# Kernel tuning notes

Measured on AMD Instinct MI355X. Metric: run time of the kernel, lower is better.

## Reference

```python
import jax, jax.numpy as jnp
import numpy as np
import math

B, L = 4, 4096
D_MODEL = 1024
D_INNER = 1024          # expand=1
D_STATE = 1             # required by rearrange 'b d 1 l' in ssm()
D_CONV = 2
DT_RANK = 64            # ceil(1024/16)
EPS = 1e-5


def setup_inputs() -> dict:
    key = jax.random.key(0)
    ks = jax.random.split(key, 8)
    dt_min, dt_max, dt_floor = 1e-3, 1e-1, 1e-4
    # dt_proj bias init: inverse-softplus of log-uniform dt (faithful to dt_init)
    dt = jnp.exp(jax.random.uniform(ks[5], (D_INNER,)) * (math.log(dt_max) - math.log(dt_min)) + math.log(dt_min))
    dt = jnp.clip(dt, dt_floor, None)
    inv_dt = dt + jnp.log(-jnp.expm1(-dt))
    std = DT_RANK ** -0.5
    return {
        "x": jax.random.normal(ks[0], (B, L, D_MODEL), dtype=jnp.float32),
        "w_in": jax.random.normal(ks[1], (2 * D_INNER, D_MODEL), dtype=jnp.float32) * 0.02,
        "conv_w": jax.random.normal(ks[2], (D_INNER, 1, D_CONV), dtype=jnp.float32) * 0.5,
        "conv_b": jnp.zeros((D_INNER,), dtype=jnp.float32),
        "x_proj_weight": jax.random.normal(ks[3], (DT_RANK + 2 * D_STATE, D_INNER), dtype=jnp.float32) * 0.02,
        "dt_projs_weight": jax.random.uniform(ks[4], (D_INNER, DT_RANK), minval=-std, maxval=std, dtype=jnp.float32),
        "dt_projs_bias": inv_dt,
        "A_logs": jnp.tile(jnp.log(jnp.arange(1, D_STATE + 1, dtype=jnp.float32))[None, :], (D_INNER, 1)),
        "Ds": jnp.ones((D_INNER,), dtype=jnp.float32),
        "ln_w": jnp.ones((D_INNER,), dtype=jnp.float32),
        "ln_b": jnp.zeros((D_INNER,), dtype=jnp.float32),
        "w_out": jax.random.normal(ks[6], (D_MODEL, D_INNER), dtype=jnp.float32) * 0.02,
    }


def _selective_scan(u, delta, A, Bs):
    # u, delta: (B, D, L); A: (D, N); Bs: (B, N, L) -> hidden states h: (B, D, N, L)
    dA = jnp.exp(jnp.einsum('bdl,dn->bdnl', delta, A))            # (B,D,N,L)
    dBu = jnp.einsum('bdl,bnl,bdl->bdnl', delta, Bs, u)           # delta * B * u
    dA_t = jnp.moveaxis(dA, -1, 0)                                # (L,B,D,N)
    dBu_t = jnp.moveaxis(dBu, -1, 0)

    def step(h, inp):
        a_t, bu_t = inp
        h = a_t * h + bu_t
        return h, h

    h0 = jnp.zeros(dA.shape[:-1], dtype=u.dtype)
    _, hs = jax.lax.scan(step, h0, (dA_t, dBu_t))                 # (L,B,D,N)
    return jnp.moveaxis(hs, 0, -1)                                # (B,D,N,L)


def reference(x, w_in, conv_w, conv_b, x_proj_weight, dt_projs_weight,
              dt_projs_bias, A_logs, Ds, ln_w, ln_b, w_out):
    Bsz, Lsz, _ = x.shape
    # in_proj (bias=False), chunk into x and gate z
    xz = x @ w_in.T                                               # (B,L,2*D)
    xc, z = xz[..., :D_INNER], xz[..., D_INNER:]
    xc = jnp.transpose(xc, (0, 2, 1))                             # (B,D,L)
    # depthwise causal conv1d, padding=d_conv-1, truncated to L
    xc = jax.lax.conv_general_dilated(
        xc, conv_w, window_strides=(1,), padding=[(D_CONV - 1, D_CONV - 1)],
        feature_group_count=D_INNER,
        dimension_numbers=('NCH', 'OIH', 'NCH'))[..., :Lsz]
    xc = xc + conv_b[None, :, None]
    xc = jax.nn.silu(xc)
    # ssm()
    x_dbl = jnp.einsum('rd,bdl->brl', x_proj_weight, xc)          # (B,R+2N,L)
    dts = x_dbl[:, :DT_RANK]
    Bs = x_dbl[:, DT_RANK:DT_RANK + D_STATE]                      # (B,N,L)
    Cs = x_dbl[:, DT_RANK + D_STATE:]                             # (B,N,L)
    dts = jnp.einsum('dr,brl->bdl', dt_projs_weight, dts)         # (B,D,L)
    A = -jnp.exp(A_logs)                                          # (D,N)
    delta = jax.nn.softplus(dts + dt_projs_bias[None, :, None])   # delta_softplus=True
    h = _selective_scan(xc, delta, A, Bs)                         # (B,D,N,L)
    h = h.reshape(Bsz, D_INNER * D_STATE, Lsz)                    # 'b d 1 l -> b (d 1) l' (N==1)
    y = h * Cs + xc * Ds[:, None]                                 # (B,D,L)
    # out_norm (LayerNorm over d_inner), gate, out_proj
    y = jnp.transpose(y, (0, 2, 1))                               # (B,L,D)
    mu = jnp.mean(y, axis=-1, keepdims=True)
    var = jnp.mean(jnp.square(y - mu), axis=-1, keepdims=True)
    y = (y - mu) * jax.lax.rsqrt(var + EPS) * ln_w + ln_b
    y = y * jax.nn.silu(z)
    return y @ w_out.T                                            # (B,L,d_model)
```

## Files before the change

kernel.cpp:

```cpp
#include <hip/hip_runtime.h>
#include <hip/hip_bf16.h>
#include <cstdint>
#include <cstddef>

typedef short short8 __attribute__((ext_vector_type(8)));
typedef short short4v __attribute__((ext_vector_type(4)));
typedef float floatx4 __attribute__((ext_vector_type(4)));

constexpr int Bz = 4;
constexpr int Lz = 4096;
constexpr int Dm = 1024;
constexpr int Di = 1024;
constexpr int Mrows = Bz * Lz;
constexpr int CH  = 32;
constexpr int NCH = Lz / CH;
constexpr int XPJ_KS = 4;

__device__ __forceinline__ void load16(const void* g, void* l) {
  __builtin_amdgcn_global_load_lds((__attribute__((address_space(1))) void*)g,
                                   (__attribute__((address_space(3))) void*)l,
                                   16, 0, 0);
}

__device__ __forceinline__ float bf2f(const __hip_bfloat16 v) { return __bfloat162float(v); }
__device__ __forceinline__ short f2bfs(float v) {
  __hip_bfloat16 h = __float2bfloat16(v);
  return *(short*)&h;
}

__global__ __launch_bounds__(256) void cvt_all(
    const float* __restrict__ x, const float* __restrict__ w_in,
    const float* __restrict__ w_out, const float* __restrict__ xpw,
    const float* __restrict__ dtw,
    __hip_bfloat16* __restrict__ xbf, __hip_bfloat16* __restrict__ w_in_bf,
    __hip_bfloat16* __restrict__ w_out_bf, __hip_bfloat16* __restrict__ xpw_bf,
    __hip_bfloat16* __restrict__ dtw_bf)
{
  const int i = blockIdx.x * 256 + threadIdx.x;
  const float* src; __hip_bfloat16* dst; int j;
  if (i < 4194304)      { src = x;     dst = xbf;      j = i; }
  else if (i < 4718592) { src = w_in;  dst = w_in_bf;  j = i - 4194304; }
  else if (i < 4980736) { src = w_out; dst = w_out_bf; j = i - 4718592; }
  else if (i < 4997632) { src = xpw;   dst = xpw_bf;   j = i - 4980736; }
  else if (i < 5014016) { src = dtw;   dst = dtw_bf;   j = i - 4997632; }
  else return;
  const float4 v = ((const float4*)src)[j];
  short4v s;
  s[0] = f2bfs(v.x); s[1] = f2bfs(v.y); s[2] = f2bfs(v.z); s[3] = f2bfs(v.w);
  ((short4v*)dst)[j] = s;
}

template <int EPI>
__global__ __launch_bounds__(256) void gemm128(
    const __hip_bfloat16* __restrict__ A,
    const __hip_bfloat16* __restrict__ W,
    int K, int N,
    __hip_bfloat16* __restrict__ outb0,
    __hip_bfloat16* __restrict__ outb1,
    float* __restrict__ outf,
    const float* __restrict__ biasf)
{
  constexpr int BK = 32;
  constexpr int GY = 16;
  __shared__ short sA[128 * BK];
  __shared__ short sB[128 * BK];
  const int tid  = threadIdx.x;
  const int wid  = tid >> 6;
  const int lane = tid & 63;

  const int gx  = gridDim.x;
  const int id  = blockIdx.y * gx + blockIdx.x;
  const int seg = gx * GY;
  const int bx  = (id % seg) / GY;
  const int by  = (id / seg) * GY + (id % GY);

  const int m0 = by * 128;
  const int n0 = bx * 128;
  const int wm = (wid & 1) * 64;
  const int wn = (wid >> 1) * 64;

  floatx4 acc[4][4];
#pragma unroll
  for (int i = 0; i < 4; i++)
#pragma unroll
    for (int j = 0; j < 4; j++) acc[i][j] = (floatx4){0.f, 0.f, 0.f, 0.f};

  const short* Ag = (const short*)A + (size_t)(m0 + (tid >> 2)) * K + (tid & 3) * 8;
  const short* Bg = (const short*)W + (size_t)(n0 + (tid >> 2)) * K + (tid & 3) * 8;
  short* sAd = &sA[tid * 8];
  short* sBd = &sB[tid * 8];
  const size_t rstep = (size_t)64 * K;
  const int fr = lane & 15, fq = lane >> 4;

  for (int kb = 0; kb < K; kb += BK) {
    load16(Ag, sAd);
    load16(Ag + rstep, sAd + 2048);
    load16(Bg, sBd);
    load16(Bg + rstep, sBd + 2048);
    Ag += BK; Bg += BK;
    __syncthreads();

    short8 av[4], bv[4];
#pragma unroll
    for (int mt = 0; mt < 4; mt++) av[mt] = *(const short8*)&sA[(wm + mt * 16 + fr) * BK + fq * 8];
#pragma unroll
    for (int nt = 0; nt < 4; nt++) bv[nt] = *(const short8*)&sB[(wn + nt * 16 + fr) * BK + fq * 8];
#pragma unroll
    for (int mt = 0; mt < 4; mt++)
#pragma unroll
      for (int nt = 0; nt < 4; nt++)
        acc[mt][nt] = __builtin_amdgcn_mfma_f32_16x16x32_bf16(av[mt], bv[nt], acc[mt][nt], 0, 0, 0);
    __syncthreads();
  }

#pragma unroll
  for (int mt = 0; mt < 4; mt++) {
#pragma unroll
    for (int nt = 0; nt < 4; nt++) {
#pragma unroll
      for (int r = 0; r < 4; r++) {
        const int gm = m0 + wm + mt * 16 + fq * 4 + r;
        const int gn = n0 + wn + nt * 16 + fr;
        float v = acc[mt][nt][r];
        if constexpr (EPI == 0) {
          if (gn < 1024) outb0[(size_t)gm * 1024 + gn] = __float2bfloat16(v);
          else           outb1[(size_t)gm * 1024 + (gn - 1024)] = __float2bfloat16(v);
        } else if constexpr (EPI == 1) {
          v += biasf[gn];
          v = (v > 15.f) ? v : __logf(1.f + __expf(v));
          outb0[(size_t)gm * N + gn] = __float2bfloat16(v);
        } else {
          outf[(size_t)gm * N + gn] = v;
        }
      }
    }
  }
}

__device__ __forceinline__ void wait_lgkm0() {
  asm volatile("s_waitcnt lgkmcnt(0)");
  __builtin_amdgcn_sched_barrier(0);
}

template <int EPI>
__device__ __forceinline__ void cluster_mfma(int MQ, floatx4 (&acc)[8][4],
                                             const short8 (&av)[8][2],
                                             const short8 (&bv)[4][2])
{
  __builtin_amdgcn_s_setprio(1);
#pragma unroll
  for (int j = 0; j < 2; j++)
#pragma unroll
    for (int nf = 0; nf < 4; nf++)
#pragma unroll
      for (int ks = 0; ks < 2; ks++)
        acc[2 * MQ + j][nf] = __builtin_amdgcn_mfma_f32_16x16x32_bf16(
            av[2 * MQ + j][ks], bv[nf][ks], acc[2 * MQ + j][nf], 0, 0, 0);
  __builtin_amdgcn_s_setprio(0);
}

template <int EPI>
__global__ __launch_bounds__(512, 2) void gemm256(
    const __hip_bfloat16* __restrict__ A,
    const __hip_bfloat16* __restrict__ W,
    int K, int N,
    __hip_bfloat16* __restrict__ outb0,
    __hip_bfloat16* __restrict__ outb1,
    float* __restrict__ outf)
{
  __shared__ alignas(16) char lds[131072];
  const int tid  = threadIdx.x;
  const int wid  = tid >> 6;
  const int lane = tid & 63;
  const int wm = wid >> 2;
  const int wn = wid & 3;
  const int fr = lane & 15, fq = lane >> 4;

  const int gx   = gridDim.x;
  const int nwg  = gx * gridDim.y;
  const int orig = blockIdx.y * gx + blockIdx.x;
  const int swz  = (orig & 7) * (nwg >> 3) + (orig >> 3);
  const int bx   = swz % gx;
  const int by   = swz / gx;
  const int m0 = by * 256;
  const int n0 = bx * 256;
  const size_t K2 = (size_t)K * 2;

  int rowo[2], colo[2];
#pragma unroll
  for (int i = 0; i < 2; i++) {
    const int p = i * 8192 + tid * 16;
    const int s = p >> 10;
    const int r = (p >> 6) & 15;
    rowo[i] = (s >> 1) * 16 + r;
    colo[i] = (s & 1) * 64 + ((p & 63) ^ (((r >> 3) & 1) << 5));
  }
  const char* Ab = (const char*)A + (size_t)m0 * K2;
  const char* Bb = (const char*)W + (size_t)n0 * K2;
  char* lbase = (char*)lds;

#define STAGE_A(c, h, kt) do {                                                          \
    load16(Ab + (size_t)((h) * 128 + rowo[0]) * K2 + (size_t)(kt) * 128 + colo[0],      \
           lbase + (c) * 32768 + (h) * 16384 + tid * 16);                               \
    load16(Ab + (size_t)((h) * 128 + rowo[1]) * K2 + (size_t)(kt) * 128 + colo[1],      \
           lbase + (c) * 32768 + (h) * 16384 + 8192 + tid * 16);                        \
  } while (0)
#define STAGE_B(c, h, kt) do {                                                          \
    load16(Bb + (size_t)((h) * 128 + rowo[0]) * K2 + (size_t)(kt) * 128 + colo[0],      \
           lbase + 65536 + (c) * 32768 + (h) * 16384 + tid * 16);                       \
    load16(Bb + (size_t)((h) * 128 + rowo[1]) * K2 + (size_t)(kt) * 128 + colo[1],      \
           lbase + 65536 + (c) * 32768 + (h) * 16384 + 8192 + tid * 16);                \
  } while (0)

  const int foff = (fr * 64 + fq * 16) ^ (((fr >> 3) & 1) << 5);

  floatx4 acc[8][4];
#pragma unroll
  for (int i = 0; i < 8; i++)
#pragma unroll
    for (int j = 0; j < 4; j++) acc[i][j] = (floatx4){0.f, 0.f, 0.f, 0.f};

  STAGE_A(0, 0, 0); STAGE_A(0, 1, 0); STAGE_B(0, 0, 0); STAGE_B(0, 1, 0);
  STAGE_B(1, 0, 1); STAGE_B(1, 1, 1); STAGE_A(1, 0, 1);
  asm volatile("s_waitcnt vmcnt(6)");
  __builtin_amdgcn_sched_barrier(0);
  __builtin_amdgcn_s_barrier();

  const int NT = K >> 6;
  short8 av[8][2], bv[4][2];
#pragma unroll 2
  for (int t = 0; t < NT; ++t) {
    const int cur = t & 1, nxt = cur ^ 1;
    const char* la = lbase + cur * 32768 + wm * 16384 + foff;
    const char* lb = lbase + 65536 + cur * 32768 + (wn >> 1) * 16384 + (wn & 1) * 8192 + foff;

#pragma unroll
    for (int nf = 0; nf < 4; nf++)
#pragma unroll
      for (int ks = 0; ks < 2; ks++)
        bv[nf][ks] = *(const short8*)(lb + (nf * 2 + ks) * 1024);
#pragma unroll
    for (int mf = 0; mf < 2; mf++)
#pragma unroll
      for (int ks = 0; ks < 2; ks++)
        av[mf][ks] = *(const short8*)(la + (mf * 2 + ks) * 1024);
    if (t + 1 < NT) STAGE_A(nxt, 1, t + 1);
    wait_lgkm0();
    cluster_mfma<EPI>(0, acc, av, bv);
    __builtin_amdgcn_s_barrier();

#pragma unroll
    for (int mf = 2; mf < 4; mf++)
#pragma unroll
      for (int ks = 0; ks < 2; ks++)
        av[mf][ks] = *(const short8*)(la + (mf * 2 + ks) * 1024);
    if (t + 2 < NT) STAGE_B(cur, 0, t + 2);
    wait_lgkm0();
    cluster_mfma<EPI>(1, acc, av, bv);
    __builtin_amdgcn_s_barrier();

#pragma unroll
    for (int mf = 4; mf < 8; mf++)
#pragma unroll
      for (int ks = 0; ks < 2; ks++)
        av[mf][ks] = *(const short8*)(la + (mf * 2 + ks) * 1024);
    if (t + 2 < NT) STAGE_B(cur, 1, t + 2);
    wait_lgkm0();
    cluster_mfma<EPI>(2, acc, av, bv);
    __builtin_amdgcn_s_barrier();

    if (t + 2 < NT) STAGE_A(cur, 0, t + 2);
    cluster_mfma<EPI>(3, acc, av, bv);
    if (t < NT - 2) {
      asm volatile("s_waitcnt vmcnt(6)");
      __builtin_amdgcn_sched_barrier(0);
      __builtin_amdgcn_s_barrier();
    } else if (t == NT - 2) {
      asm volatile("s_waitcnt vmcnt(0)");
      __builtin_amdgcn_sched_barrier(0);
      __builtin_amdgcn_s_barrier();
    }
  }
#undef STAGE_A
#undef STAGE_B

#pragma unroll
  for (int mf = 0; mf < 8; mf++) {
#pragma unroll
    for (int nf = 0; nf < 4; nf++) {
#pragma unroll
      for (int r = 0; r < 4; r++) {
        const int gm = m0 + wm * 128 + mf * 16 + fq * 4 + r;
        const int gn = n0 + wn * 64 + nf * 16 + fr;
        const float v = acc[mf][nf][r];
        if constexpr (EPI == 0) {
          if (gn < 1024) outb0[(size_t)gm * 1024 + gn] = __float2bfloat16(v);
          else           outb1[(size_t)gm * 1024 + (gn - 1024)] = __float2bfloat16(v);
        } else {
          outf[(size_t)gm * N + gn] = v;
        }
      }
    }
  }
}

__global__ __launch_bounds__(256) void gemm_xproj(
    const __hip_bfloat16* __restrict__ A,
    const __hip_bfloat16* __restrict__ W,
    float* __restrict__ part)
{
  constexpr int K = 1024, BK = 32, KC = K / XPJ_KS;
  __shared__ short sA[128 * BK];
  __shared__ short sB[80 * BK];
  const int tid = threadIdx.x;
  const int wid = tid >> 6, lane = tid & 63;
  const int kc = blockIdx.x;
  const int m0 = blockIdx.y * 128;

  floatx4 acc[2][5];
#pragma unroll
  for (int i = 0; i < 2; i++)
#pragma unroll
    for (int j = 0; j < 5; j++) acc[i][j] = (floatx4){0.f, 0.f, 0.f, 0.f};

  const short* Ag = (const short*)A + (size_t)(m0 + (tid >> 2)) * K + kc * KC + (tid & 3) * 8;
  const int brow2 = 64 + (tid >> 2);
  const int brow2c = brow2 > 65 ? 65 : brow2;
  const short* Bg  = (const short*)W + (size_t)(tid >> 2) * K + kc * KC + (tid & 3) * 8;
  const short* Bg2 = (const short*)W + (size_t)brow2c * K + kc * KC + (tid & 3) * 8;
  const size_t rstep = (size_t)64 * K;
  const int fr = lane & 15, fq = lane >> 4;

  for (int kb = 0; kb < KC; kb += BK) {
    load16(Ag, &sA[tid * 8]);
    load16(Ag + rstep, &sA[2048 + tid * 8]);
    load16(Bg, &sB[tid * 8]);
    if (tid < 64) load16(Bg2, &sB[2048 + tid * 8]);
    Ag += BK; Bg += BK; Bg2 += BK;
    __syncthreads();

    short8 av[2], bv[5];
#pragma unroll
    for (int mt = 0; mt < 2; mt++) av[mt] = *(const short8*)&sA[(wid * 32 + mt * 16 + fr) * BK + fq * 8];
#pragma unroll
    for (int nt = 0; nt < 5; nt++) bv[nt] = *(const short8*)&sB[(nt * 16 + fr) * BK + fq * 8];
#pragma unroll
    for (int mt = 0; mt < 2; mt++)
#pragma unroll
      for (int nt = 0; nt < 5; nt++)
        acc[mt][nt] = __builtin_amdgcn_mfma_f32_16x16x32_bf16(av[mt], bv[nt], acc[mt][nt], 0, 0, 0);
    __syncthreads();
  }

  float* pp = part + (size_t)kc * Mrows * 66;
#pragma unroll
  for (int mt = 0; mt < 2; mt++) {
#pragma unroll
    for (int nt = 0; nt < 5; nt++) {
#pragma unroll
      for (int r = 0; r < 4; r++) {
        const int gm = m0 + wid * 32 + mt * 16 + fq * 4 + r;
        const int gn = nt * 16 + fr;
        if (gn < 66) pp[(size_t)gm * 66 + gn] = acc[mt][nt][r];
      }
    }
  }
}

__global__ __launch_bounds__(256) void xproj_reduce(
    const float* __restrict__ part,
    __hip_bfloat16* __restrict__ dts,
    float* __restrict__ Bs, float* __restrict__ Cs)
{
  const int i = blockIdx.x * 256 + threadIdx.x;
  if (i >= Mrows * 66) return;
  const int gm = i / 66, gn = i - gm * 66;
  float s = part[i] + part[i + (size_t)Mrows * 66]
          + part[i + (size_t)2 * Mrows * 66] + part[i + (size_t)3 * Mrows * 66];
  if (gn < 64)       dts[(size_t)gm * 64 + gn] = __float2bfloat16(s);
  else if (gn == 64) Bs[gm] = s;
  else               Cs[gm] = s;
}

__global__ __launch_bounds__(256) void conv_silu(
    const __hip_bfloat16* __restrict__ xc, const float* __restrict__ cw,
    const float* __restrict__ cb, __hip_bfloat16* __restrict__ u)
{
  const size_t i8 = ((size_t)blockIdx.x * 256 + threadIdx.x) * 8;
  const int d8 = (int)(i8 & (Di - 1));
  const int l  = (int)((i8 >> 10) & (Lz - 1));
  const short8 cur = *(const short8*)((const short*)xc + i8);
  short8 prv;
  if (l > 0) prv = *(const short8*)((const short*)xc + i8 - Di);
  else       prv = (short8){0, 0, 0, 0, 0, 0, 0, 0};
  const float4* cw4 = (const float4*)(cw + 2 * d8);
  const float4 wA = cw4[0], wB = cw4[1], wC = cw4[2], wD = cw4[3];
  const float w0a[8] = {wA.x, wA.z, wB.x, wB.z, wC.x, wC.z, wD.x, wD.z};
  const float w1a[8] = {wA.y, wA.w, wB.y, wB.w, wC.y, wC.w, wD.y, wD.w};
  const float4* cb4 = (const float4*)(cb + d8);
  const float4 b0 = cb4[0], b1 = cb4[1];
  const float ba[8] = {b0.x, b0.y, b0.z, b0.w, b1.x, b1.y, b1.z, b1.w};
  short8 out;
#pragma unroll
  for (int k = 0; k < 8; k++) {
    const float pc = __uint_as_float(((uint32_t)(uint16_t)prv[k]) << 16);
    const float cc = __uint_as_float(((uint32_t)(uint16_t)cur[k]) << 16);
    const float v = pc * w0a[k] + cc * w1a[k] + ba[k];
    const float s = v / (1.f + __expf(-v));
    out[k] = f2bfs(s);
  }
  *(short8*)((short*)u + i8) = out;
}

__global__ __launch_bounds__(256) void scan_p1(
    const __hip_bfloat16* __restrict__ delta, const __hip_bfloat16* __restrict__ u,
    const float* __restrict__ Bsv, const float* __restrict__ A_logs,
    float* __restrict__ carryP, float* __restrict__ carryS)
{
  const int dp = blockIdx.x * 256 + threadIdx.x;
  const int d  = dp * 2;
  const int c = blockIdx.y, b = blockIdx.z;
  const float2 Al = *(const float2*)(A_logs + d);
  const float Ac0 = -__expf(Al.x), Ac1 = -__expf(Al.y);
  const size_t base = ((size_t)(b * Lz + c * CH)) * Di + d;
  const float* Bp = Bsv + (size_t)b * Lz + c * CH;
  float P0 = 1.f, h0 = 0.f, P1 = 1.f, h1 = 0.f;
#pragma unroll 8
  for (int j = 0; j < CH; j++) {
    const uint32_t dv = *(const uint32_t*)((const uint16_t*)delta + base + (size_t)j * Di);
    const uint32_t uv = *(const uint32_t*)((const uint16_t*)u + base + (size_t)j * Di);
    const float dl0 = __uint_as_float(dv << 16);
    const float dl1 = __uint_as_float(dv & 0xffff0000u);
    const float uu0 = __uint_as_float(uv << 16);
    const float uu1 = __uint_as_float(uv & 0xffff0000u);
    const float bj  = Bp[j];
    const float a0 = __expf(dl0 * Ac0), a1 = __expf(dl1 * Ac1);
    h0 = a0 * h0 + dl0 * bj * uu0;
    h1 = a1 * h1 + dl1 * bj * uu1;
    P0 *= a0; P1 *= a1;
  }
  const size_t ci = ((size_t)(b * NCH + c)) * Di + d;
  *(float2*)(carryP + ci) = make_float2(P0, P1);
  *(float2*)(carryS + ci) = make_float2(h0, h1);
}

__global__ __launch_bounds__(64) void scan_p2(
    const float* __restrict__ carryP, const float* __restrict__ carryS,
    float* __restrict__ hin)
{
  const int t = blockIdx.x * 64 + threadIdx.x;
  const int b = t >> 10, d = t & (Di - 1);
  float h = 0.f;
  for (int c = 0; c < NCH; c++) {
    const size_t ci = ((size_t)(b * NCH + c)) * Di + d;
    hin[ci] = h;
    h = carryP[ci] * h + carryS[ci];
  }
}

__global__ __launch_bounds__(256) void scan_p3(
    const __hip_bfloat16* __restrict__ delta, __hip_bfloat16* __restrict__ uy,
    const float* __restrict__ Bsv, const float* __restrict__ Csv,
    const float* __restrict__ A_logs, const float* __restrict__ Ds,
    const float* __restrict__ hin)
{
  const int dp = blockIdx.x * 256 + threadIdx.x;
  const int d  = dp * 2;
  const int c = blockIdx.y, b = blockIdx.z;
  const float2 Al = *(const float2*)(A_logs + d);
  const float Ac0 = -__expf(Al.x), Ac1 = -__expf(Al.y);
  const float2 Dd = *(const float2*)(Ds + d);
  const size_t base = ((size_t)(b * Lz + c * CH)) * Di + d;
  const float* Bp = Bsv + (size_t)b * Lz + c * CH;
  const float* Cp = Csv + (size_t)b * Lz + c * CH;
  const size_t ci = ((size_t)(b * NCH + c)) * Di + d;
  const float2 hh = *(const float2*)(hin + ci);
  float h0 = hh.x, h1 = hh.y;
#pragma unroll 8
  for (int j = 0; j < CH; j++) {
    const size_t ix = base + (size_t)j * Di;
    const uint32_t dv = *(const uint32_t*)((const uint16_t*)delta + ix);
    const uint32_t uv = *(const uint32_t*)((const uint16_t*)uy + ix);
    const float dl0 = __uint_as_float(dv << 16);
    const float dl1 = __uint_as_float(dv & 0xffff0000u);
    const float uu0 = __uint_as_float(uv << 16);
    const float uu1 = __uint_as_float(uv & 0xffff0000u);
    const float bj = Bp[j], cj = Cp[j];
    const float a0 = __expf(dl0 * Ac0), a1 = __expf(dl1 * Ac1);
    h0 = a0 * h0 + dl0 * bj * uu0;
    h1 = a1 * h1 + dl1 * bj * uu1;
    const float y0 = h0 * cj + uu0 * Dd.x;
    const float y1 = h1 * cj + uu1 * Dd.y;
    const uint32_t o = (uint32_t)(uint16_t)f2bfs(y0) | ((uint32_t)(uint16_t)f2bfs(y1) << 16);
    *(uint32_t*)((uint16_t*)uy + ix) = o;
  }
}

__global__ __launch_bounds__(256) void ln_gate(
    const __hip_bfloat16* __restrict__ y, const __hip_bfloat16* __restrict__ z,
    const float* __restrict__ lnw, const float* __restrict__ lnb,
    __hip_bfloat16* __restrict__ yg)
{
  const int row = blockIdx.x;
  const int tid = threadIdx.x;
  const int wid = tid >> 6, lane = tid & 63;
  const short4v yv = *(const short4v*)((const short*)y + (size_t)row * Di + tid * 4);
  const short4v zv4 = *(const short4v*)((const short*)z + (size_t)row * Di + tid * 4);
  float v[4];
#pragma unroll
  for (int i = 0; i < 4; i++)
    v[i] = __uint_as_float(((uint32_t)(uint16_t)yv[i]) << 16);
  float s1 = v[0] + v[1] + v[2] + v[3];
  float s2 = v[0] * v[0] + v[1] * v[1] + v[2] * v[2] + v[3] * v[3];
#pragma unroll
  for (int o = 32; o > 0; o >>= 1) {
    s1 += __shfl_down(s1, o, 64);
    s2 += __shfl_down(s2, o, 64);
  }
  __shared__ float r1[4], r2[4];
  if (lane == 0) { r1[wid] = s1; r2[wid] = s2; }
  __syncthreads();
  const float t1 = r1[0] + r1[1] + r1[2] + r1[3];
  const float t2 = r2[0] + r2[1] + r2[2] + r2[3];
  const float mu = t1 * (1.f / Di);
  const float var = t2 * (1.f / Di) - mu * mu;
  const float rstd = rsqrtf(var + 1e-5f);

  const float4 wv = ((const float4*)lnw)[tid];
  const float4 bv = ((const float4*)lnb)[tid];
  const float wa[4] = {wv.x, wv.y, wv.z, wv.w};
  const float ba[4] = {bv.x, bv.y, bv.z, bv.w};
  short4v og;
#pragma unroll
  for (int i = 0; i < 4; i++) {
    const float zz = __uint_as_float(((uint32_t)(uint16_t)zv4[i]) << 16);
    const float g = zz / (1.f + __expf(-zz));
    og[i] = f2bfs(((v[i] - mu) * rstd * wa[i] + ba[i]) * g);
  }
  *(short4v*)((short*)yg + (size_t)row * Di + tid * 4) = og;
}

__global__ __launch_bounds__(256) void fill_diag(float* __restrict__ out, int n, float val)
{
  const int i = blockIdx.x * 256 + threadIdx.x;
  if (i < n) out[i] = val;
}

extern "C" void kernel_launch(void* const* d_in, const int* in_sizes, int n_in,
                              void* d_out, int out_size, void* d_ws, size_t ws_size,
                              hipStream_t stream)
{
  const float* x      = (const float*)d_in[0];
  const float* w_in   = (const float*)d_in[1];
  const float* conv_w = (const float*)d_in[2];
  const float* conv_b = (const float*)d_in[3];
  const float* xpw    = (const float*)d_in[4];
  const float* dtw    = (const float*)d_in[5];
  const float* dtb    = (const float*)d_in[6];
  const float* A_logs = (const float*)d_in[7];
  const float* Ds     = (const float*)d_in[8];
  const float* lnw    = (const float*)d_in[9];
  const float* lnb    = (const float*)d_in[10];
  const float* w_out  = (const float*)d_in[11];
  float* outF = (float*)d_out;

  const size_t BF16BIG  = (size_t)Mrows * Di * sizeof(__hip_bfloat16);
  const size_t NEED_RUN = 69603328;

  if (ws_size < NEED_RUN) {
    fill_diag<<<(out_size + 255) / 256, 256, 0, stream>>>(
        outF, out_size, (float)(ws_size >> 10));
    return;
  }

  uint8_t* ws = (uint8_t*)d_ws;
  size_t off = 0;
  auto alloc = [&](size_t bytes) { void* p = ws + off; off += (bytes + 255) & ~(size_t)255; return p; };

  __hip_bfloat16* slotA    = (__hip_bfloat16*)alloc(BF16BIG);
  __hip_bfloat16* slotC    = (__hip_bfloat16*)alloc(BF16BIG);
  __hip_bfloat16* w_out_bf = (__hip_bfloat16*)alloc((size_t)Dm * Di * 2);
  __hip_bfloat16* xpw_bf   = (__hip_bfloat16*)alloc((size_t)66 * Di * 2);
  __hip_bfloat16* dtw_bf   = (__hip_bfloat16*)alloc((size_t)Di * 64 * 2);
  float* Bsv = (float*)alloc((size_t)Mrows * sizeof(float));
  float* Csv = (float*)alloc((size_t)Mrows * sizeof(float));

  __hip_bfloat16* zbuf    = (__hip_bfloat16*)d_out;
  __hip_bfloat16* w_in_bf = (__hip_bfloat16*)((uint8_t*)d_out + 33554432);
  __hip_bfloat16* dts     = (__hip_bfloat16*)((uint8_t*)d_out + 37748736);
  float* carryP = (float*)((uint8_t*)d_out + 39845888);
  float* carryS = (float*)((uint8_t*)d_out + 41943040);
  float* hin    = (float*)((uint8_t*)d_out + 44040192);
  float* xpj_part = (float*)((uint8_t*)d_out + 41943040);

  __hip_bfloat16* xbf   = slotC;
  __hip_bfloat16* xcbuf = slotA;
  __hip_bfloat16* ubuf  = slotC;
  __hip_bfloat16* delta = slotA;
  __hip_bfloat16* yg    = slotA;

  cvt_all<<<(5014016 + 255) / 256, 256, 0, stream>>>(
      x, w_in, w_out, xpw, dtw, xbf, w_in_bf, w_out_bf, xpw_bf, dtw_bf);

  gemm256<0><<<dim3(2 * Di / 256, Mrows / 256), 512, 0, stream>>>(
      xbf, w_in_bf, Dm, 2 * Di, xcbuf, zbuf, nullptr);
  conv_silu<<<(Mrows * Di / 8) / 256, 256, 0, stream>>>(xcbuf, conv_w, conv_b, ubuf);
  gemm_xproj<<<dim3(XPJ_KS, Mrows / 128), 256, 0, stream>>>(ubuf, xpw_bf, xpj_part);
  xproj_reduce<<<(Mrows * 66 + 255) / 256, 256, 0, stream>>>(xpj_part, dts, Bsv, Csv);
  gemm128<1><<<dim3(Di / 128, Mrows / 128), 256, 0, stream>>>(
      dts, dtw_bf, 64, Di, delta, nullptr, nullptr, dtb);
  scan_p1<<<dim3(Di / 512, NCH, Bz), 256, 0, stream>>>(delta, ubuf, Bsv, A_logs, carryP, carryS);
  scan_p2<<<(Bz * Di) / 64, 64, 0, stream>>>(carryP, carryS, hin);
  scan_p3<<<dim3(Di / 512, NCH, Bz), 256, 0, stream>>>(delta, ubuf, Bsv, Csv, A_logs, Ds, hin);
  ln_gate<<<Mrows, 256, 0, stream>>>(ubuf, zbuf, lnw, lnb, yg);
  gemm256<1><<<dim3(Dm / 256, Mrows / 256), 512, 0, stream>>>(
      yg, w_out_bf, Di, Dm, nullptr, nullptr, outF);
}
```

Baseline: 351.9 us.

## Fuse causal conv and SiLU into in-projection GEMM epilogue with boundary fixup

The in-projection GEMM epilogue now stages the xc half of each 256x256 tile in LDS as bf16, applies the depthwise 2-tap conv plus SiLU row by row, and writes u directly. This removes the separate full-size conv_silu pass that read xc and wrote u. Each tile's first and last rows are saved to small side buffers so a tiny conv_fix kernel can recompute the first row of every tile using the previous tile's last row. The cost is a longer epilogue that does LDS round-trips and synchronisation inside the GEMM, plus an extra small launch.

```diff
diff --git a/kernel.cpp b/kernel.cpp
--- a/kernel.cpp
+++ b/kernel.cpp
@@ -166,7 +166,9 @@
     int K, int N,
     __hip_bfloat16* __restrict__ outb0,
     __hip_bfloat16* __restrict__ outb1,
-    float* __restrict__ outf)
+    float* __restrict__ outf,
+    const float* __restrict__ cw, const float* __restrict__ cb,
+    __hip_bfloat16* __restrict__ xef, __hip_bfloat16* __restrict__ xel)
 {
   __shared__ alignas(16) char lds[131072];
   const int tid  = threadIdx.x;
@@ -284,24 +286,102 @@
 #undef STAGE_A
 #undef STAGE_B
 
-#pragma unroll
-  for (int mf = 0; mf < 8; mf++) {
-#pragma unroll
-    for (int nf = 0; nf < 4; nf++) {
-#pragma unroll
-      for (int r = 0; r < 4; r++) {
-        const int gm = m0 + wm * 128 + mf * 16 + fq * 4 + r;
-        const int gn = n0 + wn * 64 + nf * 16 + fr;
-        const float v = acc[mf][nf][r];
-        if constexpr (EPI == 0) {
-          if (gn < 1024) outb0[(size_t)gm * 1024 + gn] = __float2bfloat16(v);
-          else           outb1[(size_t)gm * 1024 + (gn - 1024)] = __float2bfloat16(v);
-        } else {
-          outf[(size_t)gm * N + gn] = v;
+  if constexpr (EPI == 0) {
+    if (n0 < 1024) {
+      short* lt = (short*)lds;
+#pragma unroll
+      for (int mf = 0; mf < 8; mf++)
+#pragma unroll
+        for (int nf = 0; nf < 4; nf++)
+#pragma unroll
+          for (int r = 0; r < 4; r++)
+            lt[(wm * 128 + mf * 16 + fq * 4 + r) * 256 + wn * 64 + nf * 16 + fr] =
+                f2bfs(acc[mf][nf][r]);
+      __syncthreads();
+
+      const int lrow0 = wid * 2 + (lane >> 5);
+      const int c8 = (lane & 31) * 8;
+      const int d0 = n0 + c8;
+      const float4* cw4 = (const float4*)(cw + 2 * d0);
+      const float4 wA = cw4[0], wB = cw4[1], wC = cw4[2], wD = cw4[3];
+      const float w0a[8] = {wA.x, wA.z, wB.x, wB.z, wC.x, wC.z, wD.x, wD.z};
+      const float w1a[8] = {wA.y, wA.w, wB.y, wB.w, wC.y, wC.w, wD.y, wD.w};
+      const float4* cb4 = (const float4*)(cb + d0);
+      const float4 b0 = cb4[0], b1 = cb4[1];
+      const float ba[8] = {b0.x, b0.y, b0.z, b0.w, b1.x, b1.y, b1.z, b1.w};
+      const int tix = m0 >> 8;
+
+      for (int it = 0; it < 16; ++it) {
+        const int rl = lrow0 + it * 16;
+        const short8 curv = *(const short8*)&lt[rl * 256 + c8];
+        if (rl == 0)   *(short8*)((short*)xef + tix * 1024 + d0) = curv;
+        if (rl == 255) *(short8*)((short*)xel + tix * 1024 + d0) = curv;
+        if (rl == 0) continue;
+        const short8 prvv = *(const short8*)&lt[(rl - 1) * 256 + c8];
+        short8 outv;
+#pragma unroll
+        for (int k = 0; k < 8; k++) {
+          const float pc = __uint_as_float(((uint32_t)(uint16_t)prvv[k]) << 16);
+          const float cc = __uint_as_float(((uint32_t)(uint16_t)curv[k]) << 16);
+          const float v = pc * w0a[k] + cc * w1a[k] + ba[k];
+          outv[k] = f2bfs(v / (1.f + __expf(-v)));
         }
+        *(short8*)((short*)outb0 + (size_t)(m0 + rl) * 1024 + d0) = outv;
       }
+    } else {
+#pragma unroll
+      for (int mf = 0; mf < 8; mf++)
+#pragma unroll
+        for (int nf = 0; nf < 4; nf++)
+#pragma unroll
+          for (int r = 0; r < 4; r++) {
+            const int gm = m0 + wm * 128 + mf * 16 + fq * 4 + r;
+            const int gn = n0 + wn * 64 + nf * 16 + fr;
+            outb1[(size_t)gm * 1024 + (gn - 1024)] = __float2bfloat16(acc[mf][nf][r]);
+          }
     }
-  }
+  } else {
+#pragma unroll
+    for (int mf = 0; mf < 8; mf++)
+#pragma unroll
+      for (int nf = 0; nf < 4; nf++)
+#pragma unroll
+        for (int r = 0; r < 4; r++) {
+          const int gm = m0 + wm * 128 + mf * 16 + fq * 4 + r;
+          const int gn = n0 + wn * 64 + nf * 16 + fr;
+          outf[(size_t)gm * N + gn] = acc[mf][nf][r];
+        }
+  }
+}
+
+__global__ __launch_bounds__(256) void conv_fix(
+    const __hip_bfloat16* __restrict__ xef, const __hip_bfloat16* __restrict__ xel,
+    const float* __restrict__ cw, const float* __restrict__ cb,
+    __hip_bfloat16* __restrict__ u)
+{
+  const int i8 = (blockIdx.x * 256 + threadIdx.x) * 8;
+  const int T  = i8 >> 10;
+  const int d0 = i8 & 1023;
+  const short8 cur = *(const short8*)((const short*)xef + T * 1024 + d0);
+  short8 prv;
+  if (T & 15) prv = *(const short8*)((const short*)xel + (T - 1) * 1024 + d0);
+  else        prv = (short8){0, 0, 0, 0, 0, 0, 0, 0};
+  const float4* cw4 = (const float4*)(cw + 2 * d0);
+  const float4 wA = cw4[0], wB = cw4[1], wC = cw4[2], wD = cw4[3];
+  const float w0a[8] = {wA.x, wA.z, wB.x, wB.z, wC.x, wC.z, wD.x, wD.z};
+  const float w1a[8] = {wA.y, wA.w, wB.y, wB.w, wC.y, wC.w, wD.y, wD.w};
+  const float4* cb4 = (const float4*)(cb + d0);
+  const float4 b0 = cb4[0], b1 = cb4[1];
+  const float ba[8] = {b0.x, b0.y, b0.z, b0.w, b1.x, b1.y, b1.z, b1.w};
+  short8 outv;
+#pragma unroll
+  for (int k = 0; k < 8; k++) {
+    const float pc = __uint_as_float(((uint32_t)(uint16_t)prv[k]) << 16);
+    const float cc = __uint_as_float(((uint32_t)(uint16_t)cur[k]) << 16);
+    const float v = pc * w0a[k] + cc * w1a[k] + ba[k];
+    outv[k] = f2bfs(v / (1.f + __expf(-v)));
+  }
+  *(short8*)((short*)u + (size_t)T * 256 * 1024 + d0) = outv;
 }
 
 __global__ __launch_bounds__(256) void gemm_xproj(
@@ -380,36 +460,6 @@
   if (gn < 64)       dts[(size_t)gm * 64 + gn] = __float2bfloat16(s);
   else if (gn == 64) Bs[gm] = s;
   else               Cs[gm] = s;
-}
-
-__global__ __launch_bounds__(256) void conv_silu(
-    const __hip_bfloat16* __restrict__ xc, const float* __restrict__ cw,
-    const float* __restrict__ cb, __hip_bfloat16* __restrict__ u)
-{
-  const size_t i8 = ((size_t)blockIdx.x * 256 + threadIdx.x) * 8;
-  const int d8 = (int)(i8 & (Di - 1));
-  const int l  = (int)((i8 >> 10) & (Lz - 1));
-  const short8 cur = *(const short8*)((const short*)xc + i8);
-  short8 prv;
-  if (l > 0) prv = *(const short8*)((const short*)xc + i8 - Di);
-  else       prv = (short8){0, 0, 0, 0, 0, 0, 0, 0};
-  const float4* cw4 = (const float4*)(cw + 2 * d8);
-  const float4 wA = cw4[0], wB = cw4[1], wC = cw4[2], wD = cw4[3];
-  const float w0a[8] = {wA.x, wA.z, wB.x, wB.z, wC.x, wC.z, wD.x, wD.z};
-  const float w1a[8] = {wA.y, wA.w, wB.y, wB.w, wC.y, wC.w, wD.y, wD.w};
-  const float4* cb4 = (const float4*)(cb + d8);
-  const float4 b0 = cb4[0], b1 = cb4[1];
-  const float ba[8] = {b0.x, b0.y, b0.z, b0.w, b1.x, b1.y, b1.z, b1.w};
-  short8 out;
-#pragma unroll
-  for (int k = 0; k < 8; k++) {
-    const float pc = __uint_as_float(((uint32_t)(uint16_t)prv[k]) << 16);
-    const float cc = __uint_as_float(((uint32_t)(uint16_t)cur[k]) << 16);
-    const float v = pc * w0a[k] + cc * w1a[k] + ba[k];
-    const float s = v / (1.f + __expf(-v));
-    out[k] = f2bfs(s);
-  }
-  *(short8*)((short*)u + i8) = out;
 }
 
 __global__ __launch_bounds__(256) void scan_p1(
@@ -591,20 +641,21 @@
   float* carryP = (float*)((uint8_t*)d_out + 39845888);
   float* carryS = (float*)((uint8_t*)d_out + 41943040);
   float* hin    = (float*)((uint8_t*)d_out + 44040192);
+  __hip_bfloat16* xef = (__hip_bfloat16*)((uint8_t*)d_out + 46137344);
+  __hip_bfloat16* xel = (__hip_bfloat16*)((uint8_t*)d_out + 46137344 + 131072);
   float* xpj_part = (float*)((uint8_t*)d_out + 41943040);
 
   __hip_bfloat16* xbf   = slotC;
-  __hip_bfloat16* xcbuf = slotA;
-  __hip_bfloat16* ubuf  = slotC;
-  __hip_bfloat16* delta = slotA;
-  __hip_bfloat16* yg    = slotA;
+  __hip_bfloat16* ubuf  = slotA;
+  __hip_bfloat16* delta = slotC;
+  __hip_bfloat16* yg    = slotC;
 
   cvt_all<<<(5014016 + 255) / 256, 256, 0, stream>>>(
       x, w_in, w_out, xpw, dtw, xbf, w_in_bf, w_out_bf, xpw_bf, dtw_bf);
 
   gemm256<0><<<dim3(2 * Di / 256, Mrows / 256), 512, 0, stream>>>(
-      xbf, w_in_bf, Dm, 2 * Di, xcbuf, zbuf, nullptr);
-  conv_silu<<<(Mrows * Di / 8) / 256, 256, 0, stream>>>(xcbuf, conv_w, conv_b, ubuf);
+      xbf, w_in_bf, Dm, 2 * Di, ubuf, zbuf, nullptr, conv_w, conv_b, xef, xel);
+  conv_fix<<<32, 256, 0, stream>>>(xef, xel, conv_w, conv_b, ubuf);
   gemm_xproj<<<dim3(XPJ_KS, Mrows / 128), 256, 0, stream>>>(ubuf, xpw_bf, xpj_part);
   xproj_reduce<<<(Mrows * 66 + 255) / 256, 256, 0, stream>>>(xpj_part, dts, Bsv, Csv);
   gemm128<1><<<dim3(Di / 128, Mrows / 128), 256, 0, stream>>>(
@@ -614,5 +665,5 @@
   scan_p3<<<dim3(Di / 512, NCH, Bz), 256, 0, stream>>>(delta, ubuf, Bsv, Csv, A_logs, Ds, hin);
   ln_gate<<<Mrows, 256, 0, stream>>>(ubuf, zbuf, lnw, lnb, yg);
   gemm256<1><<<dim3(Dm / 256, Mrows / 256), 512, 0, stream>>>(
-      yg, w_out_bf, Di, Dm, nullptr, nullptr, outF);
-}
+      yg, w_out_bf, Di, Dm, nullptr, nullptr, outF, nullptr, nullptr, nullptr, nullptr);
+}
```

New measurement: 351.2 us. No clear change (-0.2%).
